# Performance work log

Hardware: AMD Instinct MI355X
Metric: run time of the kernel (lower is better)

The kernel has to match this reference:

```python
import jax, jax.numpy as jnp
import numpy as np

D_MODEL = 1024
D_HEAD = 512
EPS = 1e-6


def setup_inputs() -> dict:
    key = jax.random.key(0)
    ks = jax.random.split(key, 12)
    s = 0.02
    B, T = 8, 2048
    return {
        "x": jax.random.normal(ks[0], (B, T, D_MODEL), dtype=jnp.float32),
        "norm_w": jnp.ones((D_MODEL,), dtype=jnp.float32),
        "Wq": jax.random.normal(ks[1], (D_HEAD, D_MODEL), dtype=jnp.float32) * s,
        "Wk": jax.random.normal(ks[2], (D_HEAD, D_MODEL), dtype=jnp.float32) * s,
        "Wv": jax.random.normal(ks[3], (D_HEAD, D_MODEL), dtype=jnp.float32) * s,
        "wi_w": jax.random.normal(ks[4], (1, D_MODEL), dtype=jnp.float32) * s,
        "wi_b": jnp.zeros((1,), dtype=jnp.float32),
        "wf_w": jax.random.normal(ks[5], (1, D_MODEL), dtype=jnp.float32) * s,
        "wf_b": jnp.zeros((1,), dtype=jnp.float32),
        "Wo": jax.random.normal(ks[6], (D_HEAD, D_MODEL), dtype=jnp.float32) * s,
        "bo": jnp.zeros((D_HEAD,), dtype=jnp.float32),
        "Wout": jax.random.normal(ks[7], (D_MODEL, D_HEAD), dtype=jnp.float32) * s,
    }


def _forward(x, norm_w, Wq, Wk, Wv, wi_w, wi_b, wf_w, wf_b, Wo, bo, Wout):
    B, T, d_model = x.shape
    d = Wq.shape[0]
    scale = 1.0 / jnp.sqrt(jnp.asarray(d, x.dtype))

    # RMSNorm (pre-norm)
    normed = x * jax.lax.rsqrt(jnp.mean(x * x, axis=-1, keepdims=True) + EPS) * norm_w

    # Precompute all per-timestep projections (vectorized over T)
    q = jnp.einsum('btm,dm->btd', normed, Wq) * scale  # (B,T,d)
    k = jnp.einsum('btm,dm->btd', normed, Wk) * scale
    v = jnp.einsum('btm,dm->btd', normed, Wv)
    zi = jnp.einsum('btm,m->bt', normed, wi_w[0]) + wi_b[0]  # (B,T)
    zf = jnp.einsum('btm,m->bt', normed, wf_w[0]) + wf_b[0]
    o = jax.nn.sigmoid(jnp.einsum('btm,dm->btd', normed, Wo) + bo)  # (B,T,d)

    # Time-major for scan
    qT = jnp.moveaxis(q, 1, 0)
    kT = jnp.moveaxis(k, 1, 0)
    vT = jnp.moveaxis(v, 1, 0)
    ziT = jnp.moveaxis(zi, 1, 0)
    zfT = jnp.moveaxis(zf, 1, 0)
    oT = jnp.moveaxis(o, 1, 0)

    C0 = jnp.zeros((B, d, d), x.dtype)
    n0 = jnp.zeros((B, d), x.dtype)
    m0 = jnp.full((B,), -jnp.inf, x.dtype)

    def step(carry, inp):
        C, n, m = carry
        q_t, k_t, v_t, zi_t, zf_t, o_t = inp
        m_t = jnp.maximum(zf_t + m, zi_t)                      # (B,)
        i_p = jnp.exp(zi_t - m_t)
        f_p = jnp.exp(zf_t + m - m_t)
        C_t = f_p[:, None, None] * C + i_p[:, None, None] * (v_t[:, :, None] * k_t[:, None, :])
        n_t = f_p[:, None] * n + i_p[:, None] * k_t
        Cq = jnp.einsum('bij,bj->bi', C_t, q_t)                # (B,d)
        denom = jnp.maximum(jnp.abs(jnp.sum(n_t * q_t, axis=-1, keepdims=True)), 1.0)
        h = o_t * Cq / denom
        return (C_t, n_t, m_t), h

    (C_f, n_f, m_f), hT = jax.lax.scan(step, (C0, n0, m0), (qT, kT, vT, ziT, zfT, oT))
    h = jnp.moveaxis(hT, 0, 1)                                 # (B,T,d)
    out = x + jnp.einsum('btd,md->btm', h, Wout)
    return out


def reference(x, norm_w, Wq, Wk, Wv, wi_w, wi_b, wf_w, wf_b, Wo, bo, Wout):
    return _forward(x, norm_w, Wq, Wk, Wv, wi_w, wi_b, wf_w, wf_b, Wo, bo, Wout)
```

## Files before the change

### kernel.cpp

```cpp
#include <hip/hip_runtime.h>
#include <cstdint>
#include <cmath>

#define T_SEQ 2048
#define NBATCH 8
#define DM 1024
#define DH 512
#define MROWS (NBATCH * T_SEQ)
#define NC 16
#define CL 128

typedef short s8v __attribute__((ext_vector_type(8)));
typedef float f32x4 __attribute__((ext_vector_type(4)));

typedef unsigned int __attribute__((address_space(1))) uint_g;
typedef unsigned int __attribute__((address_space(3))) uint_l;

#define QKSCALE 0.044194173824159216f

__device__ __forceinline__ float b2f(unsigned short s) {
    union { unsigned u; float f; } c; c.u = ((unsigned)s) << 16; return c.f;
}
__device__ __forceinline__ unsigned short f2b(float f) {
    union { float f; unsigned u; } c; c.f = f;
    unsigned r = c.u + 0x7fffu + ((c.u >> 16) & 1u);
    return (unsigned short)(r >> 16);
}
__device__ __forceinline__ void gld_lds16(const void* g, void* l) {
    __builtin_amdgcn_global_load_lds((const uint_g*)g, (uint_l*)l, 16, 0, 0);
}

#define WAITV(N) asm volatile("s_waitcnt vmcnt(" #N ")" ::: "memory")
#define BARSYNC() do { asm volatile("" ::: "memory"); __builtin_amdgcn_s_barrier(); asm volatile("" ::: "memory"); } while (0)

__global__ __launch_bounds__(256) void norm_kernel(
    const float* __restrict__ x, const float* __restrict__ nw,
    const float* __restrict__ wi, const float* __restrict__ wf,
    const float* __restrict__ wib, const float* __restrict__ wfb,
    unsigned short* __restrict__ normed, float* __restrict__ zi, float* __restrict__ zf,
    const float* __restrict__ Wq, const float* __restrict__ Wk,
    const float* __restrict__ Wo, const float* __restrict__ Wv,
    const float* __restrict__ Wout,
    unsigned short* __restrict__ Wcat1, unsigned short* __restrict__ WvB,
    unsigned short* __restrict__ Woutb)
{
    int t = blockIdx.x, tid = threadIdx.x;
    float4 xv = ((const float4*)(x + (size_t)t * DM))[tid];
    float ss = xv.x * xv.x + xv.y * xv.y + xv.z * xv.z + xv.w * xv.w;
#pragma unroll
    for (int m = 1; m < 64; m <<= 1) ss += __shfl_xor(ss, m, 64);
    __shared__ float sred[4];
    __shared__ float sred2[8];
    if ((tid & 63) == 0) sred[tid >> 6] = ss;
    __syncthreads();
    ss = sred[0] + sred[1] + sred[2] + sred[3];
    float rstd = rsqrtf(ss * (1.0f / DM) + 1e-6f);
    float4 nwv = ((const float4*)nw)[tid];
    float n0 = xv.x * rstd * nwv.x, n1 = xv.y * rstd * nwv.y;
    float n2 = xv.z * rstd * nwv.z, n3 = xv.w * rstd * nwv.w;
    ushort4 pk;
    pk.x = f2b(n0); pk.y = f2b(n1); pk.z = f2b(n2); pk.w = f2b(n3);
    ((ushort4*)(normed + (size_t)t * DM))[tid] = pk;
    float4 wiv = ((const float4*)wi)[tid];
    float4 wfv = ((const float4*)wf)[tid];
    float pzi = n0 * wiv.x + n1 * wiv.y + n2 * wiv.z + n3 * wiv.w;
    float pzf = n0 * wfv.x + n1 * wfv.y + n2 * wfv.z + n3 * wfv.w;
#pragma unroll
    for (int m = 1; m < 64; m <<= 1) {
        pzi += __shfl_xor(pzi, m, 64);
        pzf += __shfl_xor(pzf, m, 64);
    }
    if ((tid & 63) == 0) { sred2[tid >> 6] = pzi; sred2[4 + (tid >> 6)] = pzf; }
    __syncthreads();
    if (tid == 0) {
        zi[t] = sred2[0] + sred2[1] + sred2[2] + sred2[3] + wib[0];
        zf[t] = sred2[4] + sred2[5] + sred2[6] + sred2[7] + wfb[0];
    }
    if (tid < 160) {
        int idx = blockIdx.x * 160 + tid;
        if (idx < 1572864) {
            int nrow = idx >> 10;
            float v;
            if      (nrow < 512)  v = Wq[idx];
            else if (nrow < 1024) v = Wk[idx - 512 * 1024];
            else                  v = Wo[idx - 1024 * 1024];
            Wcat1[idx] = f2b(v);
        } else if (idx < 2097152) {
            int j = idx - 1572864;
            WvB[j] = f2b(Wv[j]);
        } else {
            int j = idx - 2097152;
            Woutb[j] = f2b(Wout[j]);
        }
    }
}

__global__ __launch_bounds__(256) void mscan2_kernel(
    const float* __restrict__ zi, const float* __restrict__ zf,
    float* __restrict__ u, float* __restrict__ a)
{
    int b = blockIdx.x, tid = threadIdx.x, lane = tid & 63, wid = tid >> 6;
    size_t base = (size_t)b * T_SEQ + tid * 8;
    float z_f[8], z_i[8];
    *(float4*)&z_f[0] = *(const float4*)&zf[base];
    *(float4*)&z_f[4] = *(const float4*)&zf[base + 4];
    *(float4*)&z_i[0] = *(const float4*)&zi[base];
    *(float4*)&z_i[4] = *(const float4*)&zi[base + 4];
    __shared__ float wt[4];
    float c8[8]; float run = 0.0f;
#pragma unroll
    for (int i = 0; i < 8; ++i) { run += z_f[i]; c8[i] = run; }
    float v = run;
#pragma unroll
    for (int d = 1; d < 64; d <<= 1) {
        float o = __shfl_up(v, d, 64);
        if (lane >= d) v += o;
    }
    if (lane == 63) wt[wid] = v;
    __syncthreads();
    float woff = 0.0f;
    for (int j = 0; j < wid; ++j) woff += wt[j];
    float excl = __shfl_up(v, 1, 64);
    if (lane == 0) excl = 0.0f;
    float pre = woff + excl;
    float uu[8];
#pragma unroll
    for (int i = 0; i < 8; ++i) uu[i] = z_i[i] - (pre + c8[i]);
    *(float4*)&u[base] = *(float4*)&uu[0];
    *(float4*)&u[base + 4] = *(float4*)&uu[4];
    __syncthreads();
    float m8[8]; float rm = -INFINITY;
#pragma unroll
    for (int i = 0; i < 8; ++i) { rm = fmaxf(rm, uu[i]); m8[i] = rm; }
    float mv = rm;
#pragma unroll
    for (int d = 1; d < 64; d <<= 1) {
        float o = __shfl_up(mv, d, 64);
        if (lane >= d) mv = fmaxf(mv, o);
    }
    if (lane == 63) wt[wid] = mv;
    __syncthreads();
    float moff = -INFINITY;
    for (int j = 0; j < wid; ++j) moff = fmaxf(moff, wt[j]);
    float mexcl = __shfl_up(mv, 1, 64);
    if (lane == 0) mexcl = -INFINITY;
    float mpre = fmaxf(moff, mexcl);
    float aa[8];
#pragma unroll
    for (int i = 0; i < 8; ++i) aa[i] = fmaxf(mpre, m8[i]);
    *(float4*)&a[base] = *(float4*)&aa[0];
    *(float4*)&a[base + 4] = *(float4*)&aa[4];
}

__global__ __launch_bounds__(256, 4) void gemm_qkv(
    const unsigned short* __restrict__ normed, const unsigned short* __restrict__ Wcat1,
    const unsigned short* __restrict__ WvB, int K,
    unsigned short* __restrict__ qko, const float* __restrict__ bo,
    unsigned short* __restrict__ vout)
{
    __shared__ unsigned short As[128 * 64];
    __shared__ unsigned short Bs[128 * 64];
    int tid = threadIdx.x;
    int l = tid & 63, w = tid >> 6;
    int wg = (blockIdx.x & 7) * 256 + (blockIdx.x >> 3);
    int job = (wg >= 1536) ? 1 : 0;
    const unsigned short* A;
    const unsigned short* Bw;
    int bm, bn;
    if (job == 0) { A = normed; Bw = Wcat1; bn = wg % 12; bm = wg / 12; }
    else          { int w2 = wg - 1536; A = WvB; Bw = normed; bm = w2 & 3; bn = w2 >> 2; }
    int wr = w >> 1, wc = w & 1;
    f32x4 acc[4][4] = {};
    const size_t abase = (size_t)(bm * 128) * K;
    const size_t bbase = (size_t)(bn * 128) * K;

    for (int ks = 0; ks < K; ks += 64) {
        __syncthreads();
#pragma unroll
        for (int i = 0; i < 4; ++i) {
            int off = (i * 256 + tid) * 8;
            int row = off >> 6, kc = off & 63;
            int kcs = kc ^ ((row & 7) << 3);
            gld_lds16(A + abase + (size_t)row * K + ks + kcs, &As[off]);
            gld_lds16(Bw + bbase + (size_t)row * K + ks + kcs, &Bs[off]);
        }
        __syncthreads();
#pragma unroll
        for (int kk = 0; kk < 2; ++kk) {
            int cbo = kk * 32 + (l >> 4) * 8;
            s8v af[4], bfv[4];
#pragma unroll
            for (int m = 0; m < 4; ++m) {
                int row = wr * 64 + m * 16 + (l & 15);
                af[m] = *(const s8v*)&As[row * 64 + (cbo ^ ((row & 7) << 3))];
            }
#pragma unroll
            for (int n = 0; n < 4; ++n) {
                int row = wc * 64 + n * 16 + (l & 15);
                bfv[n] = *(const s8v*)&Bs[row * 64 + (cbo ^ ((row & 7) << 3))];
            }
#pragma unroll
            for (int m = 0; m < 4; ++m)
#pragma unroll
                for (int n = 0; n < 4; ++n)
                    acc[m][n] = __builtin_amdgcn_mfma_f32_16x16x32_bf16(af[m], bfv[n], acc[m][n], 0, 0, 0);
        }
    }

    if (job == 0) {
#pragma unroll
        for (int m = 0; m < 4; ++m) {
#pragma unroll
            for (int n = 0; n < 4; ++n) {
                int col = bn * 128 + wc * 64 + n * 16 + (l & 15);
#pragma unroll
                for (int r = 0; r < 4; ++r) {
                    int row = bm * 128 + wr * 64 + m * 16 + (l >> 4) * 4 + r;
                    float v = acc[m][n][r];
                    if (col < 1024) v *= QKSCALE;
                    else {
                        float s = v + bo[col - 1024];
                        v = 1.0f / (1.0f + expf(-s));
                    }
                    qko[(size_t)row * 1536 + col] = f2b(v);
                }
            }
        }
    } else {
#pragma unroll
        for (int m = 0; m < 4; ++m) {
#pragma unroll
            for (int n = 0; n < 4; ++n) {
                int col = bn * 128 + wc * 64 + n * 16 + (l & 15);
#pragma unroll
                for (int r = 0; r < 4; ++r) {
                    int row = bm * 128 + wr * 64 + m * 16 + (l >> 4) * 4 + r;
                    vout[(size_t)row * MROWS + col] = f2b(acc[m][n][r]);
                }
            }
        }
    }
}

template <int EPI, int ORD>
__global__ __launch_bounds__(256, 4) void gemm_bt(
    const unsigned short* __restrict__ A, const unsigned short* __restrict__ Bw,
    int M, int N, int K, int ldo,
    unsigned short* __restrict__ outb, const float* __restrict__ bo,
    float* __restrict__ outf, const float* __restrict__ xres)
{
    __shared__ unsigned short As[128 * 64];
    __shared__ unsigned short Bs[128 * 64];
    int tid = threadIdx.x;
    int l = tid & 63, w = tid >> 6;
    int cpx = gridDim.x >> 3;
    int wg = (blockIdx.x & 7) * cpx + (blockIdx.x >> 3);
    int mb = M >> 7;
    int nb = N >> 7;
    int bm, bn;
    if (ORD == 0) { bm = wg % mb; bn = wg / mb; }
    else          { bn = wg % nb; bm = wg / nb; }
    int wr = w >> 1, wc = w & 1;
    f32x4 acc[4][4] = {};
    const size_t abase = (size_t)(bm * 128) * K;
    const size_t bbase = (size_t)(bn * 128) * K;

    for (int ks = 0; ks < K; ks += 64) {
        __syncthreads();
#pragma unroll
        for (int i = 0; i < 4; ++i) {
            int off = (i * 256 + tid) * 8;
            int row = off >> 6, kc = off & 63;
            int kcs = kc ^ ((row & 7) << 3);
            gld_lds16(A + abase + (size_t)row * K + ks + kcs, &As[off]);
            gld_lds16(Bw + bbase + (size_t)row * K + ks + kcs, &Bs[off]);
        }
        __syncthreads();
#pragma unroll
        for (int kk = 0; kk < 2; ++kk) {
            int cbo = kk * 32 + (l >> 4) * 8;
            s8v af[4], bfv[4];
#pragma unroll
            for (int m = 0; m < 4; ++m) {
                int row = wr * 64 + m * 16 + (l & 15);
                af[m] = *(const s8v*)&As[row * 64 + (cbo ^ ((row & 7) << 3))];
            }
#pragma unroll
            for (int n = 0; n < 4; ++n) {
                int row = wc * 64 + n * 16 + (l & 15);
                bfv[n] = *(const s8v*)&Bs[row * 64 + (cbo ^ ((row & 7) << 3))];
            }
#pragma unroll
            for (int m = 0; m < 4; ++m)
#pragma unroll
                for (int n = 0; n < 4; ++n)
                    acc[m][n] = __builtin_amdgcn_mfma_f32_16x16x32_bf16(af[m], bfv[n], acc[m][n], 0, 0, 0);
        }
    }

#pragma unroll
    for (int m = 0; m < 4; ++m) {
#pragma unroll
        for (int n = 0; n < 4; ++n) {
            int col = bn * 128 + wc * 64 + n * 16 + (l & 15);
#pragma unroll
            for (int r = 0; r < 4; ++r) {
                int row = bm * 128 + wr * 64 + m * 16 + (l >> 4) * 4 + r;
                float v = acc[m][n][r];
                if (EPI == 3) {
                    outb[(size_t)row * ldo + col] = f2b(v);
                } else {
                    size_t idx = (size_t)row * ldo + col;
                    outf[idx] = xres[idx] + v;
                }
            }
        }
    }
}

__global__ __launch_bounds__(256) void phaseA_kernel(
    const unsigned short* __restrict__ qko,
    const float* __restrict__ u, const float* __restrict__ a,
    unsigned short* __restrict__ st, float* __restrict__ rowsum)
{
    __shared__ unsigned short Qs[64 * 32], Ks[128 * 32];
    int bid = blockIdx.x;
    int b = bid & 7, c = (bid >> 3) & 15, th = bid >> 7;
    int tid = threadIdx.x, l = tid & 63, wv = tid >> 6;
    size_t cb = (size_t)b * T_SEQ + c * CL;
    f32x4 acc[8] = {};
    for (int ks = 0; ks < 512; ks += 32) {
        __syncthreads();
        {
            int p = tid;
            int row = p >> 2, kc = (p & 3) * 8;
            gld_lds16(qko + (cb + th * 64 + row) * 1536 + ks + kc, &Qs[p * 8]);
#pragma unroll
            for (int rI = 0; rI < 2; ++rI) {
                int pp = rI * 256 + tid;
                int rw = pp >> 2, kk = (pp & 3) * 8;
                gld_lds16(qko + (cb + rw) * 1536 + 512 + ks + kk, &Ks[pp * 8]);
            }
        }
        __syncthreads();
        s8v af = *(const s8v*)&Qs[(wv * 16 + (l & 15)) * 32 + (l >> 4) * 8];
#pragma unroll
        for (int n = 0; n < 8; ++n) {
            s8v bf = *(const s8v*)&Ks[(n * 16 + (l & 15)) * 32 + (l >> 4) * 8];
            acc[n] = __builtin_amdgcn_mfma_f32_16x16x32_bf16(af, bf, acc[n], 0, 0, 0);
        }
    }
    float rs[4] = {0.f, 0.f, 0.f, 0.f};
    size_t stb = (size_t)(b * NC + c) * (CL * CL);
#pragma unroll
    for (int e = 0; e < 4; ++e) {
        int tl = th * 64 + wv * 16 + (l >> 4) * 4 + e;
        float a_t = a[cb + tl];
#pragma unroll
        for (int n = 0; n < 8; ++n) {
            int j = n * 16 + (l & 15);
            float val = (j <= tl) ? acc[n][e] * expf(u[cb + j] - a_t) : 0.0f;
            rs[e] += val;
            st[stb + (size_t)tl * CL + j] = f2b(val);
        }
    }
#pragma unroll
    for (int e = 0; e < 4; ++e) {
#pragma unroll
        for (int m = 1; m < 16; m <<= 1) rs[e] += __shfl_xor(rs[e], m, 64);
    }
    if ((l & 15) == 0) {
#pragma unroll
        for (int e = 0; e < 4; ++e)
            rowsum[cb + th * 64 + wv * 16 + (l >> 4) * 4 + e] = rs[e];
    }
}

__global__ __launch_bounds__(256) void kwprep2_kernel(
    const unsigned short* __restrict__ qko,
    const float* __restrict__ u, const float* __restrict__ a,
    unsigned short* __restrict__ kw, float* __restrict__ P, float* __restrict__ aE)
{
    __shared__ unsigned short T[64][136];
    __shared__ float w_l[CL];
    int bid = blockIdx.x;
    int b = bid & 7, c = (bid >> 3) & 15, st = bid >> 7;
    int s0 = st * 64;
    int tid = threadIdx.x;
    size_t cb = (size_t)b * T_SEQ + c * CL;
    float a_e = a[cb + CL - 1];
    if (tid < CL) w_l[tid] = expf(u[cb + tid] - a_e);
    if (tid == 0 && st == 0) aE[b * NC + c] = a_e;
#pragma unroll
    for (int it = 0; it < 4; ++it) {
        int flat = it * 256 + tid;
        int t = flat >> 3, g = flat & 7;
        s8v v = *(const s8v*)&qko[(cb + t) * 1536 + 512 + s0 + g * 8];
#pragma unroll
        for (int e = 0; e < 8; ++e) T[g * 8 + e][t] = (unsigned short)v[e];
    }
    __syncthreads();
    int s = tid >> 2, tg = tid & 3;
    float psum = 0.0f;
#pragma unroll
    for (int j = 0; j < 4; ++j) {
        int t0 = tg * 32 + j * 8;
        s8v kv = *(const s8v*)&T[s][t0];
        s8v kwv;
#pragma unroll
        for (int e = 0; e < 8; ++e) {
            float f = b2f((unsigned short)kv[e]) * w_l[t0 + e];
            kwv[e] = (short)f2b(f);
            psum += f;
        }
        *(s8v*)&kw[(size_t)(s0 + s) * MROWS + cb + t0] = kwv;
    }
    psum += __shfl_xor(psum, 1, 64);
    psum += __shfl_xor(psum, 2, 64);
    if (tg == 0) P[(size_t)(b * NC + c) * 512 + s0 + s] = psum;
}

__global__ __launch_bounds__(256) void nhscan_kernel(
    const float* __restrict__ P, const float* __restrict__ aE,
    float* __restrict__ nhprev)
{
    int gid = blockIdx.x * 256 + threadIdx.x;
    int b = gid >> 9, s = gid & 511;
    float nh = 0.0f, aprev = 0.0f;
    for (int c = 0; c < NC; ++c) {
        nhprev[(size_t)(b * NC + c) * 512 + s] = nh;
        float ae = aE[b * NC + c];
        float gam = (c == 0) ? 0.0f : expf(aprev - ae);
        nh = gam * nh + P[(size_t)(b * NC + c) * 512 + s];
        aprev = ae;
    }
}

__global__ __launch_bounds__(256) void denom_kernel(
    const unsigned short* __restrict__ qko, const float* __restrict__ nhprev,
    const float* __restrict__ aE, const float* __restrict__ a,
    const float* __restrict__ rowsum, float* __restrict__ rdnm)
{
    int wv = threadIdx.x >> 6, l = threadIdx.x & 63;
    int t = blockIdx.x * 4 + wv;
    int b = t >> 11, c = (t & 2047) >> 7;
    const unsigned short* qrow = qko + (size_t)t * 1536 + l * 8;
    const float* nh = nhprev + (size_t)(b * NC + c) * 512 + l * 8;
    s8v qv = *(const s8v*)qrow;
    float4 n0 = *(const float4*)nh;
    float4 n1 = *(const float4*)(nh + 4);
    float nq = b2f((unsigned short)qv[0]) * n0.x + b2f((unsigned short)qv[1]) * n0.y
             + b2f((unsigned short)qv[2]) * n0.z + b2f((unsigned short)qv[3]) * n0.w
             + b2f((unsigned short)qv[4]) * n1.x + b2f((unsigned short)qv[5]) * n1.y
             + b2f((unsigned short)qv[6]) * n1.z + b2f((unsigned short)qv[7]) * n1.w;
#pragma unroll
    for (int m = 1; m < 64; m <<= 1) nq += __shfl_xor(nq, m, 64);
    if (l == 0) {
        float beta = (c == 0) ? 0.0f : expf(aE[b * NC + c - 1] - a[t]);
        rdnm[t] = 1.0f / fmaxf(fabsf(beta * nq + rowsum[t]), 1.0f);
    }
}

__global__ __launch_bounds__(256, 2) void cscan2_kernel(
    const unsigned short* __restrict__ kvT, const unsigned short* __restrict__ kw,
    const float* __restrict__ aE, unsigned short* __restrict__ chk)
{
    __shared__ unsigned short Vs[2][64 * 128];
    __shared__ unsigned short Ks[2][64 * 128];
    int bid = blockIdx.x;
    int b = bid & 7, rt = (bid >> 3) & 7, st = bid >> 6;
    int r0 = rt * 64, s0 = st * 64;
    int tid = threadIdx.x, l = tid & 63;
    int w = tid >> 6, wr = w >> 1, wc = w & 1;
    size_t tb = (size_t)b * T_SEQ;
    int srow = tid >> 4, sg = tid & 15;
    f32x4 acc[2][2] = {};
    float a_prev = 0.0f;

#define CSTAGE(c, buf) do { \
        size_t cb_ = tb + (size_t)(c) * CL; \
        _Pragma("unroll") \
        for (int i = 0; i < 4; ++i) { \
            int row_ = i * 16 + srow; \
            int gs_ = sg ^ (row_ & 7); \
            gld_lds16(kvT + (size_t)(512 + r0 + row_) * MROWS + cb_ + gs_ * 8, \
                      &Vs[buf][(i * 256 + tid) * 8]); \
        } \
        _Pragma("unroll") \
        for (int i = 0; i < 4; ++i) { \
            int row_ = i * 16 + srow; \
            int gs_ = sg ^ (row_ & 7); \
            gld_lds16(kw + (size_t)(s0 + row_) * MROWS + cb_ + gs_ * 8, \
                      &Ks[buf][(i * 256 + tid) * 8]); \
        } } while (0)

    CSTAGE(0, 0);
    for (int c = 0; c < NC; ++c) {
        int cur = c & 1;
        if (c + 1 < NC) { CSTAGE(c + 1, cur ^ 1); WAITV(8); }
        else            { WAITV(0); }
        BARSYNC();
        float a_e = aE[b * NC + c];
        if (c > 0) {
            unsigned short* slot = chk + (size_t)(b * (NC - 1) + (c - 1)) * (512 * 512);
#pragma unroll
            for (int m = 0; m < 2; ++m)
#pragma unroll
                for (int n = 0; n < 2; ++n)
#pragma unroll
                    for (int e = 0; e < 4; ++e) {
                        int r = r0 + wr * 32 + m * 16 + (l >> 4) * 4 + e;
                        int s = s0 + wc * 32 + n * 16 + (l & 15);
                        slot[r * 512 + s] = f2b(acc[m][n][e]);
                    }
            float gam = expf(a_prev - a_e);
#pragma unroll
            for (int m = 0; m < 2; ++m)
#pragma unroll
                for (int n = 0; n < 2; ++n)
#pragma unroll
                    for (int e = 0; e < 4; ++e) acc[m][n][e] *= gam;
        }
#pragma unroll
        for (int ks = 0; ks < 4; ++ks) {
            s8v vf[2], kf[2];
#pragma unroll
            for (int m = 0; m < 2; ++m) {
                int row = wr * 32 + m * 16 + (l & 15);
                int gf = ks * 4 + (l >> 4);
                vf[m] = *(const s8v*)&Vs[cur][row * 128 + ((gf ^ (row & 7)) << 3)];
            }
#pragma unroll
            for (int n = 0; n < 2; ++n) {
                int row = wc * 32 + n * 16 + (l & 15);
                int gf = ks * 4 + (l >> 4);
                kf[n] = *(const s8v*)&Ks[cur][row * 128 + ((gf ^ (row & 7)) << 3)];
            }
#pragma unroll
            for (int m = 0; m < 2; ++m)
#pragma unroll
                for (int n = 0; n < 2; ++n)
                    acc[m][n] = __builtin_amdgcn_mfma_f32_16x16x32_bf16(vf[m], kf[n], acc[m][n], 0, 0, 0);
        }
        a_prev = a_e;
        BARSYNC();
    }
#undef CSTAGE
}

__global__ __launch_bounds__(512) void hout_kernel(
    const unsigned short* __restrict__ qko, const unsigned short* __restrict__ kvT,
    const unsigned short* __restrict__ st, const unsigned short* __restrict__ chk,
    const float* __restrict__ a, const float* __restrict__ aE,
    const float* __restrict__ rdnm, unsigned short* __restrict__ g)
{
    int bid = blockIdx.x;
    int b = bid & 7, cc = bid >> 3;
    int c = cc >> 1, rh = cc & 1;
    int tid = threadIdx.x, l = tid & 63, wv = tid >> 6;
    int mq = wv & 3;
    int rr = (wv >> 2) * 128 + rh * 256;
    size_t cb = (size_t)b * T_SEQ + c * CL;
    f32x4 acc[2][8] = {};

    if (c > 0) {
        const unsigned short* slot = chk + (size_t)(b * (NC - 1) + (c - 1)) * (512 * 512);
#pragma unroll
        for (int ks = 0; ks < 16; ++ks) {
            s8v aq[2];
#pragma unroll
            for (int mf = 0; mf < 2; ++mf)
                aq[mf] = *(const s8v*)&qko[(cb + mq * 32 + mf * 16 + (l & 15)) * 1536 + ks * 32 + (l >> 4) * 8];
#pragma unroll
            for (int n = 0; n < 8; ++n) {
                s8v bc = *(const s8v*)&slot[(size_t)(rr + n * 16 + (l & 15)) * 512 + ks * 32 + (l >> 4) * 8];
                acc[0][n] = __builtin_amdgcn_mfma_f32_16x16x32_bf16(aq[0], bc, acc[0][n], 0, 0, 0);
                acc[1][n] = __builtin_amdgcn_mfma_f32_16x16x32_bf16(aq[1], bc, acc[1][n], 0, 0, 0);
            }
        }
        float aprev = aE[b * NC + c - 1];
#pragma unroll
        for (int mf = 0; mf < 2; ++mf)
#pragma unroll
            for (int e = 0; e < 4; ++e) {
                int t = mq * 32 + mf * 16 + (l >> 4) * 4 + e;
                float bta = expf(aprev - a[cb + t]);
#pragma unroll
                for (int n = 0; n < 8; ++n) acc[mf][n][e] *= bta;
            }
    }
    const unsigned short* stp = st + (size_t)(b * NC + c) * (CL * CL);
#pragma unroll
    for (int ks = 0; ks < 4; ++ks) {
        s8v aq[2];
#pragma unroll
        for (int mf = 0; mf < 2; ++mf)
            aq[mf] = *(const s8v*)&stp[(size_t)(mq * 32 + mf * 16 + (l & 15)) * CL + ks * 32 + (l >> 4) * 8];
#pragma unroll
        for (int n = 0; n < 8; ++n) {
            s8v bv = *(const s8v*)&kvT[(size_t)(512 + rr + n * 16 + (l & 15)) * MROWS + cb + ks * 32 + (l >> 4) * 8];
            acc[0][n] = __builtin_amdgcn_mfma_f32_16x16x32_bf16(aq[0], bv, acc[0][n], 0, 0, 0);
            acc[1][n] = __builtin_amdgcn_mfma_f32_16x16x32_bf16(aq[1], bv, acc[1][n], 0, 0, 0);
        }
    }
#pragma unroll
    for (int mf = 0; mf < 2; ++mf)
#pragma unroll
        for (int e = 0; e < 4; ++e) {
            int t = mq * 32 + mf * 16 + (l >> 4) * 4 + e;
            float rd = rdnm[cb + t];
#pragma unroll
            for (int n = 0; n < 8; ++n) {
                int r = rr + n * 16 + (l & 15);
                float ov = b2f(qko[(cb + t) * 1536 + 1024 + r]);
                g[(cb + t) * DH + r] = f2b(ov * acc[mf][n][e] * rd);
            }
        }
}

extern "C" void kernel_launch(void* const* d_in, const int* in_sizes, int n_in,
                              void* d_out, int out_size, void* d_ws, size_t ws_size,
                              hipStream_t stream)
{
    (void)in_sizes; (void)n_in; (void)out_size; (void)ws_size;
    const float* x    = (const float*)d_in[0];
    const float* nw   = (const float*)d_in[1];
    const float* Wq   = (const float*)d_in[2];
    const float* Wk   = (const float*)d_in[3];
    const float* Wv   = (const float*)d_in[4];
    const float* wi   = (const float*)d_in[5];
    const float* wib  = (const float*)d_in[6];
    const float* wf   = (const float*)d_in[7];
    const float* wfb  = (const float*)d_in[8];
    const float* Wo   = (const float*)d_in[9];
    const float* bo   = (const float*)d_in[10];
    const float* Wout = (const float*)d_in[11];
    float* out = (float*)d_out;

    char* ws = (char*)d_ws;
    unsigned short* qko    = (unsigned short*)ws;
    unsigned short* kvT    = (unsigned short*)(ws + 50331648);
    unsigned short* normed = (unsigned short*)(ws + 83886080);
    unsigned short* g      = normed;
    unsigned short* kw     = (unsigned short*)(ws + 100663296);
    float* Pbuf   = (float*)(ws + 117440512);
    float* nhprev = (float*)(ws + 117702656);
    float* aE     = (float*)(ws + 117964800);
    unsigned short* Wcat1  = (unsigned short*)(ws + 117440512);
    unsigned short* WvB    = (unsigned short*)(ws + 120586240);
    unsigned short* Woutb  = (unsigned short*)(ws + 122683392);
    float* zi     = (float*)(ws + 123731968);
    float* zf     = zi + MROWS;
    float* uarr   = zf + MROWS;
    float* aarr   = uarr + MROWS;
    float* rowsum = aarr + MROWS;
    float* rdnm   = rowsum + MROWS;

    unsigned short* chk   = (unsigned short*)d_out;
    unsigned short* stbuf = (unsigned short*)((char*)d_out + 62914560);

    norm_kernel    <<<MROWS, 256, 0, stream>>>(x, nw, wi, wf, wib, wfb, normed, zi, zf,
                                               Wq, Wk, Wo, Wv, Wout, Wcat1, WvB, Woutb);
    mscan2_kernel  <<<NBATCH, 256, 0, stream>>>(zi, zf, uarr, aarr);
    gemm_qkv       <<<2048, 256, 0, stream>>>(normed, Wcat1, WvB, DM, qko, bo, kvT + (size_t)512 * MROWS);
    phaseA_kernel  <<<256, 256, 0, stream>>>(qko, uarr, aarr, stbuf, rowsum);
    kwprep2_kernel <<<1024, 256, 0, stream>>>(qko, uarr, aarr, kw, Pbuf, aE);
    nhscan_kernel  <<<16, 256, 0, stream>>>(Pbuf, aE, nhprev);
    denom_kernel   <<<4096, 256, 0, stream>>>(qko, nhprev, aE, aarr, rowsum, rdnm);
    cscan2_kernel  <<<512, 256, 0, stream>>>(kvT, kw, aE, chk);
    hout_kernel    <<<256, 512, 0, stream>>>(qko, kvT, stbuf, chk, aarr, aE, rdnm, g);
    gemm_bt<1, 1>  <<<128 * 8, 256, 0, stream>>>(g, Woutb, MROWS, DM, DH, DM, nullptr, nullptr, out, x);
}
```

Measured before the change: 274.2 us.

## Fuse small scan and denominator kernels into neighbouring kernels to cut launches

Folds the log-gate prefix scan into extra blocks of the QKV GEMM launch and merges the intra-chunk score and key-weighting kernels into one launch with block-index dispatch. It also moves the chunk normalizer scan and the denominator computation to the tail of the chunk-state scan kernel. Each block there recomputes the prefix of P per timestep group instead of reading a precomputed buffer. This removes four kernel launches and the gaps between them, at the cost of redundant per-block recomputation and extra shared memory and register pressure in the merged kernels.

Measured after the change: 273.3 us. Within noise of the previous version (-0.3%).

```diff
diff --git a/kernel.cpp b/kernel.cpp
--- a/kernel.cpp
+++ b/kernel.cpp
@@ -95,72 +95,73 @@
     }
 }
 
-__global__ __launch_bounds__(256) void mscan2_kernel(
+__global__ __launch_bounds__(256, 4) void gemm_qkv_ms(
+    const unsigned short* __restrict__ normed, const unsigned short* __restrict__ Wcat1,
+    const unsigned short* __restrict__ WvB, int K,
+    unsigned short* __restrict__ qko, const float* __restrict__ bo,
+    unsigned short* __restrict__ vout,
     const float* __restrict__ zi, const float* __restrict__ zf,
     float* __restrict__ u, float* __restrict__ a)
 {
-    int b = blockIdx.x, tid = threadIdx.x, lane = tid & 63, wid = tid >> 6;
-    size_t base = (size_t)b * T_SEQ + tid * 8;
-    float z_f[8], z_i[8];
-    *(float4*)&z_f[0] = *(const float4*)&zf[base];
-    *(float4*)&z_f[4] = *(const float4*)&zf[base + 4];
-    *(float4*)&z_i[0] = *(const float4*)&zi[base];
-    *(float4*)&z_i[4] = *(const float4*)&zi[base + 4];
-    __shared__ float wt[4];
-    float c8[8]; float run = 0.0f;
-#pragma unroll
-    for (int i = 0; i < 8; ++i) { run += z_f[i]; c8[i] = run; }
-    float v = run;
-#pragma unroll
-    for (int d = 1; d < 64; d <<= 1) {
-        float o = __shfl_up(v, d, 64);
-        if (lane >= d) v += o;
-    }
-    if (lane == 63) wt[wid] = v;
-    __syncthreads();
-    float woff = 0.0f;
-    for (int j = 0; j < wid; ++j) woff += wt[j];
-    float excl = __shfl_up(v, 1, 64);
-    if (lane == 0) excl = 0.0f;
-    float pre = woff + excl;
-    float uu[8];
-#pragma unroll
-    for (int i = 0; i < 8; ++i) uu[i] = z_i[i] - (pre + c8[i]);
-    *(float4*)&u[base] = *(float4*)&uu[0];
-    *(float4*)&u[base + 4] = *(float4*)&uu[4];
-    __syncthreads();
-    float m8[8]; float rm = -INFINITY;
-#pragma unroll
-    for (int i = 0; i < 8; ++i) { rm = fmaxf(rm, uu[i]); m8[i] = rm; }
-    float mv = rm;
-#pragma unroll
-    for (int d = 1; d < 64; d <<= 1) {
-        float o = __shfl_up(mv, d, 64);
-        if (lane >= d) mv = fmaxf(mv, o);
-    }
-    if (lane == 63) wt[wid] = mv;
-    __syncthreads();
-    float moff = -INFINITY;
-    for (int j = 0; j < wid; ++j) moff = fmaxf(moff, wt[j]);
-    float mexcl = __shfl_up(mv, 1, 64);
-    if (lane == 0) mexcl = -INFINITY;
-    float mpre = fmaxf(moff, mexcl);
-    float aa[8];
-#pragma unroll
-    for (int i = 0; i < 8; ++i) aa[i] = fmaxf(mpre, m8[i]);
-    *(float4*)&a[base] = *(float4*)&aa[0];
-    *(float4*)&a[base + 4] = *(float4*)&aa[4];
-}
-
-__global__ __launch_bounds__(256, 4) void gemm_qkv(
-    const unsigned short* __restrict__ normed, const unsigned short* __restrict__ Wcat1,
-    const unsigned short* __restrict__ WvB, int K,
-    unsigned short* __restrict__ qko, const float* __restrict__ bo,
-    unsigned short* __restrict__ vout)
-{
     __shared__ unsigned short As[128 * 64];
     __shared__ unsigned short Bs[128 * 64];
+    __shared__ float wt[4];
     int tid = threadIdx.x;
+
+    if (blockIdx.x >= 2048) {
+        int b = blockIdx.x - 2048, lane = tid & 63, wid = tid >> 6;
+        size_t base = (size_t)b * T_SEQ + tid * 8;
+        float z_f[8], z_i[8];
+        *(float4*)&z_f[0] = *(const float4*)&zf[base];
+        *(float4*)&z_f[4] = *(const float4*)&zf[base + 4];
+        *(float4*)&z_i[0] = *(const float4*)&zi[base];
+        *(float4*)&z_i[4] = *(const float4*)&zi[base + 4];
+        float c8[8]; float run = 0.0f;
+#pragma unroll
+        for (int i = 0; i < 8; ++i) { run += z_f[i]; c8[i] = run; }
+        float v = run;
+#pragma unroll
+        for (int d = 1; d < 64; d <<= 1) {
+            float o = __shfl_up(v, d, 64);
+            if (lane >= d) v += o;
+        }
+        if (lane == 63) wt[wid] = v;
+        __syncthreads();
+        float woff = 0.0f;
+        for (int j = 0; j < wid; ++j) woff += wt[j];
+        float excl = __shfl_up(v, 1, 64);
+        if (lane == 0) excl = 0.0f;
+        float pre = woff + excl;
+        float uu[8];
+#pragma unroll
+        for (int i = 0; i < 8; ++i) uu[i] = z_i[i] - (pre + c8[i]);
+        *(float4*)&u[base] = *(float4*)&uu[0];
+        *(float4*)&u[base + 4] = *(float4*)&uu[4];
+        __syncthreads();
+        float m8[8]; float rm = -INFINITY;
+#pragma unroll
+        for (int i = 0; i < 8; ++i) { rm = fmaxf(rm, uu[i]); m8[i] = rm; }
+        float mv = rm;
+#pragma unroll
+        for (int d = 1; d < 64; d <<= 1) {
+            float o = __shfl_up(mv, d, 64);
+            if (lane >= d) mv = fmaxf(mv, o);
+        }
+        if (lane == 63) wt[wid] = mv;
+        __syncthreads();
+        float moff = -INFINITY;
+        for (int j = 0; j < wid; ++j) moff = fmaxf(moff, wt[j]);
+        float mexcl = __shfl_up(mv, 1, 64);
+        if (lane == 0) mexcl = -INFINITY;
+        float mpre = fmaxf(moff, mexcl);
+        float aa[8];
+#pragma unroll
+        for (int i = 0; i < 8; ++i) aa[i] = fmaxf(mpre, m8[i]);
+        *(float4*)&a[base] = *(float4*)&aa[0];
+        *(float4*)&a[base + 4] = *(float4*)&aa[4];
+        return;
+    }
+
     int l = tid & 63, w = tid >> 6;
     int wg = (blockIdx.x & 7) * 256 + (blockIdx.x >> 3);
     int job = (wg >= 1536) ? 1 : 0;
@@ -318,152 +319,113 @@
     }
 }
 
-__global__ __launch_bounds__(256) void phaseA_kernel(
+__global__ __launch_bounds__(256) void fusedA_kernel(
     const unsigned short* __restrict__ qko,
     const float* __restrict__ u, const float* __restrict__ a,
-    unsigned short* __restrict__ st, float* __restrict__ rowsum)
-{
-    __shared__ unsigned short Qs[64 * 32], Ks[128 * 32];
-    int bid = blockIdx.x;
-    int b = bid & 7, c = (bid >> 3) & 15, th = bid >> 7;
-    int tid = threadIdx.x, l = tid & 63, wv = tid >> 6;
-    size_t cb = (size_t)b * T_SEQ + c * CL;
-    f32x4 acc[8] = {};
-    for (int ks = 0; ks < 512; ks += 32) {
-        __syncthreads();
-        {
-            int p = tid;
-            int row = p >> 2, kc = (p & 3) * 8;
-            gld_lds16(qko + (cb + th * 64 + row) * 1536 + ks + kc, &Qs[p * 8]);
-#pragma unroll
-            for (int rI = 0; rI < 2; ++rI) {
-                int pp = rI * 256 + tid;
-                int rw = pp >> 2, kk = (pp & 3) * 8;
-                gld_lds16(qko + (cb + rw) * 1536 + 512 + ks + kk, &Ks[pp * 8]);
-            }
-        }
-        __syncthreads();
-        s8v af = *(const s8v*)&Qs[(wv * 16 + (l & 15)) * 32 + (l >> 4) * 8];
-#pragma unroll
-        for (int n = 0; n < 8; ++n) {
-            s8v bf = *(const s8v*)&Ks[(n * 16 + (l & 15)) * 32 + (l >> 4) * 8];
-            acc[n] = __builtin_amdgcn_mfma_f32_16x16x32_bf16(af, bf, acc[n], 0, 0, 0);
-        }
-    }
-    float rs[4] = {0.f, 0.f, 0.f, 0.f};
-    size_t stb = (size_t)(b * NC + c) * (CL * CL);
-#pragma unroll
-    for (int e = 0; e < 4; ++e) {
-        int tl = th * 64 + wv * 16 + (l >> 4) * 4 + e;
-        float a_t = a[cb + tl];
-#pragma unroll
-        for (int n = 0; n < 8; ++n) {
-            int j = n * 16 + (l & 15);
-            float val = (j <= tl) ? acc[n][e] * expf(u[cb + j] - a_t) : 0.0f;
-            rs[e] += val;
-            st[stb + (size_t)tl * CL + j] = f2b(val);
-        }
-    }
-#pragma unroll
-    for (int e = 0; e < 4; ++e) {
-#pragma unroll
-        for (int m = 1; m < 16; m <<= 1) rs[e] += __shfl_xor(rs[e], m, 64);
-    }
-    if ((l & 15) == 0) {
-#pragma unroll
-        for (int e = 0; e < 4; ++e)
-            rowsum[cb + th * 64 + wv * 16 + (l >> 4) * 4 + e] = rs[e];
-    }
-}
-
-__global__ __launch_bounds__(256) void kwprep2_kernel(
-    const unsigned short* __restrict__ qko,
-    const float* __restrict__ u, const float* __restrict__ a,
+    unsigned short* __restrict__ stb, float* __restrict__ rowsum,
     unsigned short* __restrict__ kw, float* __restrict__ P, float* __restrict__ aE)
 {
-    __shared__ unsigned short T[64][136];
-    __shared__ float w_l[CL];
-    int bid = blockIdx.x;
-    int b = bid & 7, c = (bid >> 3) & 15, st = bid >> 7;
-    int s0 = st * 64;
-    int tid = threadIdx.x;
-    size_t cb = (size_t)b * T_SEQ + c * CL;
-    float a_e = a[cb + CL - 1];
-    if (tid < CL) w_l[tid] = expf(u[cb + tid] - a_e);
-    if (tid == 0 && st == 0) aE[b * NC + c] = a_e;
-#pragma unroll
-    for (int it = 0; it < 4; ++it) {
-        int flat = it * 256 + tid;
-        int t = flat >> 3, g = flat & 7;
-        s8v v = *(const s8v*)&qko[(cb + t) * 1536 + 512 + s0 + g * 8];
-#pragma unroll
-        for (int e = 0; e < 8; ++e) T[g * 8 + e][t] = (unsigned short)v[e];
-    }
-    __syncthreads();
-    int s = tid >> 2, tg = tid & 3;
-    float psum = 0.0f;
-#pragma unroll
-    for (int j = 0; j < 4; ++j) {
-        int t0 = tg * 32 + j * 8;
-        s8v kv = *(const s8v*)&T[s][t0];
-        s8v kwv;
-#pragma unroll
-        for (int e = 0; e < 8; ++e) {
-            float f = b2f((unsigned short)kv[e]) * w_l[t0 + e];
-            kwv[e] = (short)f2b(f);
-            psum += f;
-        }
-        *(s8v*)&kw[(size_t)(s0 + s) * MROWS + cb + t0] = kwv;
-    }
-    psum += __shfl_xor(psum, 1, 64);
-    psum += __shfl_xor(psum, 2, 64);
-    if (tg == 0) P[(size_t)(b * NC + c) * 512 + s0 + s] = psum;
-}
-
-__global__ __launch_bounds__(256) void nhscan_kernel(
-    const float* __restrict__ P, const float* __restrict__ aE,
-    float* __restrict__ nhprev)
-{
-    int gid = blockIdx.x * 256 + threadIdx.x;
-    int b = gid >> 9, s = gid & 511;
-    float nh = 0.0f, aprev = 0.0f;
-    for (int c = 0; c < NC; ++c) {
-        nhprev[(size_t)(b * NC + c) * 512 + s] = nh;
-        float ae = aE[b * NC + c];
-        float gam = (c == 0) ? 0.0f : expf(aprev - ae);
-        nh = gam * nh + P[(size_t)(b * NC + c) * 512 + s];
-        aprev = ae;
-    }
-}
-
-__global__ __launch_bounds__(256) void denom_kernel(
-    const unsigned short* __restrict__ qko, const float* __restrict__ nhprev,
-    const float* __restrict__ aE, const float* __restrict__ a,
-    const float* __restrict__ rowsum, float* __restrict__ rdnm)
-{
-    int wv = threadIdx.x >> 6, l = threadIdx.x & 63;
-    int t = blockIdx.x * 4 + wv;
-    int b = t >> 11, c = (t & 2047) >> 7;
-    const unsigned short* qrow = qko + (size_t)t * 1536 + l * 8;
-    const float* nh = nhprev + (size_t)(b * NC + c) * 512 + l * 8;
-    s8v qv = *(const s8v*)qrow;
-    float4 n0 = *(const float4*)nh;
-    float4 n1 = *(const float4*)(nh + 4);
-    float nq = b2f((unsigned short)qv[0]) * n0.x + b2f((unsigned short)qv[1]) * n0.y
-             + b2f((unsigned short)qv[2]) * n0.z + b2f((unsigned short)qv[3]) * n0.w
-             + b2f((unsigned short)qv[4]) * n1.x + b2f((unsigned short)qv[5]) * n1.y
-             + b2f((unsigned short)qv[6]) * n1.z + b2f((unsigned short)qv[7]) * n1.w;
-#pragma unroll
-    for (int m = 1; m < 64; m <<= 1) nq += __shfl_xor(nq, m, 64);
-    if (l == 0) {
-        float beta = (c == 0) ? 0.0f : expf(aE[b * NC + c - 1] - a[t]);
-        rdnm[t] = 1.0f / fmaxf(fabsf(beta * nq + rowsum[t]), 1.0f);
-    }
-}
-
-__global__ __launch_bounds__(256, 2) void cscan2_kernel(
+    __shared__ char smem[17920];
+    int bid = blockIdx.x, tid = threadIdx.x;
+
+    if (bid < 256) {
+        unsigned short* Qs = (unsigned short*)smem;
+        unsigned short* Ks = (unsigned short*)(smem + 4096);
+        int b = bid & 7, c = (bid >> 3) & 15, th = bid >> 7;
+        int l = tid & 63, wv = tid >> 6;
+        size_t cb = (size_t)b * T_SEQ + c * CL;
+        f32x4 acc[8] = {};
+        for (int ks = 0; ks < 512; ks += 32) {
+            __syncthreads();
+            {
+                int p = tid;
+                int row = p >> 2, kc = (p & 3) * 8;
+                gld_lds16(qko + (cb + th * 64 + row) * 1536 + ks + kc, &Qs[p * 8]);
+#pragma unroll
+                for (int rI = 0; rI < 2; ++rI) {
+                    int pp = rI * 256 + tid;
+                    int rw = pp >> 2, kk = (pp & 3) * 8;
+                    gld_lds16(qko + (cb + rw) * 1536 + 512 + ks + kk, &Ks[pp * 8]);
+                }
+            }
+            __syncthreads();
+            s8v af = *(const s8v*)&Qs[(wv * 16 + (l & 15)) * 32 + (l >> 4) * 8];
+#pragma unroll
+            for (int n = 0; n < 8; ++n) {
+                s8v bf = *(const s8v*)&Ks[(n * 16 + (l & 15)) * 32 + (l >> 4) * 8];
+                acc[n] = __builtin_amdgcn_mfma_f32_16x16x32_bf16(af, bf, acc[n], 0, 0, 0);
+            }
+        }
+        float rs[4] = {0.f, 0.f, 0.f, 0.f};
+        size_t stbase = (size_t)(b * NC + c) * (CL * CL);
+#pragma unroll
+        for (int e = 0; e < 4; ++e) {
+            int tl = th * 64 + wv * 16 + (l >> 4) * 4 + e;
+            float a_t = a[cb + tl];
+#pragma unroll
+            for (int n = 0; n < 8; ++n) {
+                int j = n * 16 + (l & 15);
+                float val = (j <= tl) ? acc[n][e] * expf(u[cb + j] - a_t) : 0.0f;
+                rs[e] += val;
+                stb[stbase + (size_t)tl * CL + j] = f2b(val);
+            }
+        }
+#pragma unroll
+        for (int e = 0; e < 4; ++e) {
+#pragma unroll
+            for (int m = 1; m < 16; m <<= 1) rs[e] += __shfl_xor(rs[e], m, 64);
+        }
+        if ((l & 15) == 0) {
+#pragma unroll
+            for (int e = 0; e < 4; ++e)
+                rowsum[cb + th * 64 + wv * 16 + (l >> 4) * 4 + e] = rs[e];
+        }
+    } else {
+        unsigned short (*T)[136] = (unsigned short(*)[136])smem;
+        float* w_l = (float*)(smem + 17408);
+        int kb = bid - 256;
+        int b = kb & 7, c = (kb >> 3) & 15, stt = kb >> 7;
+        int s0 = stt * 64;
+        size_t cb = (size_t)b * T_SEQ + c * CL;
+        float a_e = a[cb + CL - 1];
+        if (tid < CL) w_l[tid] = expf(u[cb + tid] - a_e);
+        if (tid == 0 && stt == 0) aE[b * NC + c] = a_e;
+#pragma unroll
+        for (int it = 0; it < 4; ++it) {
+            int flat = it * 256 + tid;
+            int t = flat >> 3, g = flat & 7;
+            s8v v = *(const s8v*)&qko[(cb + t) * 1536 + 512 + s0 + g * 8];
+#pragma unroll
+            for (int e = 0; e < 8; ++e) T[g * 8 + e][t] = (unsigned short)v[e];
+        }
+        __syncthreads();
+        int s = tid >> 2, tg = tid & 3;
+        float psum = 0.0f;
+#pragma unroll
+        for (int j = 0; j < 4; ++j) {
+            int t0 = tg * 32 + j * 8;
+            s8v kv = *(const s8v*)&T[s][t0];
+            s8v kwv;
+#pragma unroll
+            for (int e = 0; e < 8; ++e) {
+                float f = b2f((unsigned short)kv[e]) * w_l[t0 + e];
+                kwv[e] = (short)f2b(f);
+                psum += f;
+            }
+            *(s8v*)&kw[(size_t)(s0 + s) * MROWS + cb + t0] = kwv;
+        }
+        psum += __shfl_xor(psum, 1, 64);
+        psum += __shfl_xor(psum, 2, 64);
+        if (tg == 0) P[(size_t)(b * NC + c) * 512 + s0 + s] = psum;
+    }
+}
+
+__global__ __launch_bounds__(256, 2) void cscan3_kernel(
     const unsigned short* __restrict__ kvT, const unsigned short* __restrict__ kw,
-    const float* __restrict__ aE, unsigned short* __restrict__ chk)
+    const float* __restrict__ aE, unsigned short* __restrict__ chk,
+    const unsigned short* __restrict__ qko, const float* __restrict__ P,
+    const float* __restrict__ a, const float* __restrict__ rowsum,
+    float* __restrict__ rdnm)
 {
     __shared__ unsigned short Vs[2][64 * 128];
     __shared__ unsigned short Ks[2][64 * 128];
@@ -546,6 +508,40 @@
         BARSYNC();
     }
 #undef CSTAGE
+
+    {
+        int wv = tid >> 6;
+        int t0 = bid * 32 + wv * 8;
+        int bt = t0 >> 11, ct = (t0 & 2047) >> 7;
+        float nh[8] = {0, 0, 0, 0, 0, 0, 0, 0};
+        float aprev = 0.0f;
+        for (int cp = 0; cp < ct; ++cp) {
+            float ae = aE[bt * NC + cp];
+            float gam = (cp == 0) ? 0.0f : expf(aprev - ae);
+            const float* Pp = P + (size_t)(bt * NC + cp) * 512 + l * 8;
+            float4 p0 = *(const float4*)Pp;
+            float4 p1 = *(const float4*)(Pp + 4);
+#pragma unroll
+            for (int e = 0; e < 8; ++e) nh[e] *= gam;
+            nh[0] += p0.x; nh[1] += p0.y; nh[2] += p0.z; nh[3] += p0.w;
+            nh[4] += p1.x; nh[5] += p1.y; nh[6] += p1.z; nh[7] += p1.w;
+            aprev = ae;
+        }
+        float aeprev = (ct > 0) ? aE[bt * NC + ct - 1] : 0.0f;
+        for (int tt = 0; tt < 8; ++tt) {
+            int tc = t0 + tt;
+            s8v qv = *(const s8v*)(qko + (size_t)tc * 1536 + l * 8);
+            float nq = 0.0f;
+#pragma unroll
+            for (int e = 0; e < 8; ++e) nq += b2f((unsigned short)qv[e]) * nh[e];
+#pragma unroll
+            for (int m = 1; m < 64; m <<= 1) nq += __shfl_xor(nq, m, 64);
+            if (l == 0) {
+                float beta = (ct == 0) ? 0.0f : expf(aeprev - a[tc]);
+                rdnm[tc] = 1.0f / fmaxf(fabsf(beta * nq + rowsum[tc]), 1.0f);
+            }
+        }
+    }
 }
 
 __global__ __launch_bounds__(512) void hout_kernel(
@@ -644,7 +640,6 @@
     unsigned short* g      = normed;
     unsigned short* kw     = (unsigned short*)(ws + 100663296);
     float* Pbuf   = (float*)(ws + 117440512);
-    float* nhprev = (float*)(ws + 117702656);
     float* aE     = (float*)(ws + 117964800);
     unsigned short* Wcat1  = (unsigned short*)(ws + 117440512);
     unsigned short* WvB    = (unsigned short*)(ws + 120586240);
@@ -661,13 +656,10 @@
 
     norm_kernel    <<<MROWS, 256, 0, stream>>>(x, nw, wi, wf, wib, wfb, normed, zi, zf,
                                                Wq, Wk, Wo, Wv, Wout, Wcat1, WvB, Woutb);
-    mscan2_kernel  <<<NBATCH, 256, 0, stream>>>(zi, zf, uarr, aarr);
-    gemm_qkv       <<<2048, 256, 0, stream>>>(normed, Wcat1, WvB, DM, qko, bo, kvT + (size_t)512 * MROWS);
-    phaseA_kernel  <<<256, 256, 0, stream>>>(qko, uarr, aarr, stbuf, rowsum);
-    kwprep2_kernel <<<1024, 256, 0, stream>>>(qko, uarr, aarr, kw, Pbuf, aE);
-    nhscan_kernel  <<<16, 256, 0, stream>>>(Pbuf, aE, nhprev);
-    denom_kernel   <<<4096, 256, 0, stream>>>(qko, nhprev, aE, aarr, rowsum, rdnm);
-    cscan2_kernel  <<<512, 256, 0, stream>>>(kvT, kw, aE, chk);
+    gemm_qkv_ms    <<<2056, 256, 0, stream>>>(normed, Wcat1, WvB, DM, qko, bo,
+                                              kvT + (size_t)512 * MROWS, zi, zf, uarr, aarr);
+    fusedA_kernel  <<<1280, 256, 0, stream>>>(qko, uarr, aarr, stbuf, rowsum, kw, Pbuf, aE);
+    cscan3_kernel  <<<512, 256, 0, stream>>>(kvT, kw, aE, chk, qko, Pbuf, aarr, rowsum, rdnm);
     hout_kernel    <<<256, 512, 0, stream>>>(qko, kvT, stbuf, chk, aarr, aE, rdnm, g);
     gemm_bt<1, 1>  <<<128 * 8, 256, 0, stream>>>(g, Woutb, MROWS, DM, DH, DM, nullptr, nullptr, out, x);
 }
```
